# Kernel tuning notes

Measured on AMD Instinct MI355X. Metric: run time of the kernel, lower is better.

## Reference

```python
import jax, jax.numpy as jnp
import numpy as np

B, S, D = 2, 2048, 768
H = 12
HD = D // H


def setup_inputs() -> dict:
    key = jax.random.key(0)
    k1, k2, k3 = jax.random.split(key, 3)
    hidden_states = jax.random.normal(k1, (B, S, D), dtype=jnp.float32)
    Wqkv = jax.random.normal(k2, (D, 3 * D), dtype=jnp.float32) * (1.0 / np.sqrt(D))
    bqkv = jnp.zeros((3 * D,), dtype=jnp.float32)
    Wout = jax.random.normal(k3, (D, D), dtype=jnp.float32) * (1.0 / np.sqrt(D))
    bout = jnp.zeros((D,), dtype=jnp.float32)
    return {"hidden_states": hidden_states, "Wqkv": Wqkv, "bqkv": bqkv,
            "Wout": Wout, "bout": bout}


def reference(hidden_states, Wqkv, bqkv, Wout, bout):
    b, s, d = hidden_states.shape
    h, hd = H, HD
    scale = hd ** -0.5
    qkv = hidden_states @ Wqkv + bqkv                      # [b, s, 3d]
    q, k, v = jnp.split(qkv, 3, axis=-1)
    # [b, h, s, hd]
    q = q.reshape(b, s, h, hd).transpose(0, 2, 1, 3)
    k = k.reshape(b, s, h, hd).transpose(0, 2, 1, 3)
    v = v.reshape(b, s, h, hd).transpose(0, 2, 1, 3)
    scores = jnp.einsum('bhqd,bhkd->bhqk', q, k) * scale   # [b, h, s, s]
    causal = jnp.tril(jnp.ones((s, s), dtype=bool))
    scores = jnp.where(causal, scores, -jnp.inf)
    attn = jax.nn.softmax(scores, axis=-1)
    out = jnp.einsum('bhqk,bhkd->bhqd', attn, v)           # [b, h, s, hd]
    out = out.transpose(0, 2, 1, 3).reshape(b, s, d)
    return out @ Wout + bout
```

## Files before the change

kernel.cpp:

```cpp
#include <hip/hip_runtime.h>
#include <hip/hip_bf16.h>

typedef __attribute__((ext_vector_type(8))) short bf16x8;
typedef __attribute__((ext_vector_type(4))) float f32x4;
typedef __attribute__((ext_vector_type(4))) unsigned int u32x4;

#define NB 2
#define NS 2048
#define ND 768
#define NH 12
#define NHD 64
#define N3D 2304
#define NM (NB * NS)

__device__ __forceinline__ unsigned short f2bf(float x) {
    union { float f; unsigned u; } v; v.f = x;
    unsigned r = v.u + 0x7FFFu + ((v.u >> 16) & 1u);
    return (unsigned short)(r >> 16);
}

__device__ __forceinline__ unsigned cvt_pk_bf16(float lo, float hi) {
    unsigned r;
    asm volatile("v_cvt_pk_bf16_f32 %0, %1, %2" : "=v"(r) : "v"(lo), "v"(hi));
    return r;
}

__global__ __launch_bounds__(256)
void conv_bf16(const float* __restrict__ in, unsigned short* __restrict__ out) {
    const int i = (blockIdx.x * 256 + threadIdx.x) * 4;
    float4 v = *reinterpret_cast<const float4*>(in + i);
    ushort4 o;
    o.x = f2bf(v.x); o.y = f2bf(v.y); o.z = f2bf(v.z); o.w = f2bf(v.w);
    *reinterpret_cast<ushort4*>(out + i) = o;
}

__global__ __launch_bounds__(256)
void transp_conv(const float* __restrict__ in, unsigned short* __restrict__ out,
                 int K, int N) {
    __shared__ float T[32][33];
    const int n0 = blockIdx.x * 32, k0 = blockIdx.y * 32;
    const int r = threadIdx.x >> 3, c4 = (threadIdx.x & 7) * 4;
    float4 v = *reinterpret_cast<const float4*>(&in[(size_t)(k0 + r) * N + n0 + c4]);
    T[r][c4 + 0] = v.x; T[r][c4 + 1] = v.y; T[r][c4 + 2] = v.z; T[r][c4 + 3] = v.w;
    __syncthreads();
    ushort4 o;
    o.x = f2bf(T[c4 + 0][r]); o.y = f2bf(T[c4 + 1][r]);
    o.z = f2bf(T[c4 + 2][r]); o.w = f2bf(T[c4 + 3][r]);
    *reinterpret_cast<ushort4*>(&out[(size_t)(n0 + r) * K + k0 + c4]) = o;
}

template<int BM, int EPI>
__global__ __launch_bounds__(256)
void gemm_k768(const unsigned short* __restrict__ A,
               const unsigned short* __restrict__ Bt,
               const float* __restrict__ bias,
               unsigned short* __restrict__ Qo, unsigned short* __restrict__ Ko,
               unsigned short* __restrict__ Vto, float* __restrict__ Co) {
    __shared__ unsigned short As[2][BM * 64];
    __shared__ unsigned short Bs[2][128 * 64];
    const int t = threadIdx.x;
    const int wv = t >> 6, lane = t & 63;
    const int lr = lane & 15, lg = lane >> 4;
    const int wr = wv >> 1, wc = wv & 1;
    const int m0 = blockIdx.y * BM;
    const int n0 = blockIdx.x * 128;
    constexpr int FM = BM / 32;

    f32x4 acc[FM][4];
#pragma unroll
    for (int i = 0; i < FM; ++i)
#pragma unroll
        for (int j = 0; j < 4; ++j) acc[i][j] = (f32x4){0.f, 0.f, 0.f, 0.f};

    const int sr = t >> 3;
    const int sb = t & 7;

#define GSTAGE(buf, k0)                                                          \
    {                                                                            \
        _Pragma("unroll")                                                        \
        for (int jj = 0; jj < BM / 32; ++jj) {                                   \
            const int row = jj * 32 + sr;                                        \
            __builtin_amdgcn_global_load_lds(                                    \
                (const void*)(A + (size_t)(m0 + row) * ND + (k0) + ((sb ^ (row & 7)) * 8)), \
                (void*)(As[buf] + jj * 2048 + wv * 512), 16, 0, 0);              \
        }                                                                        \
        _Pragma("unroll")                                                        \
        for (int jj = 0; jj < 4; ++jj) {                                         \
            const int row = jj * 32 + sr;                                        \
            __builtin_amdgcn_global_load_lds(                                    \
                (const void*)(Bt + (size_t)(n0 + row) * ND + (k0) + ((sb ^ (row & 7)) * 8)), \
                (void*)(Bs[buf] + jj * 2048 + wv * 512), 16, 0, 0);              \
        }                                                                        \
    }

    GSTAGE(0, 0);
    for (int ki = 0; ki < ND / 64; ++ki) {
        __syncthreads();
        if (ki + 1 < ND / 64) GSTAGE((ki + 1) & 1, (ki + 1) * 64);
        const unsigned short* Ac = As[ki & 1];
        const unsigned short* Bc = Bs[ki & 1];
#pragma unroll
        for (int kc = 0; kc < 2; ++kc) {
            bf16x8 af[FM], bfr[4];
#pragma unroll
            for (int mi = 0; mi < FM; ++mi) {
                const int row = wr * (BM / 2) + mi * 16 + lr;
                af[mi] = *(const bf16x8*)&Ac[row * 64 + (((kc * 4 + lg) ^ (row & 7)) * 8)];
            }
#pragma unroll
            for (int nj = 0; nj < 4; ++nj) {
                const int row = wc * 64 + nj * 16 + lr;
                bfr[nj] = *(const bf16x8*)&Bc[row * 64 + (((kc * 4 + lg) ^ (row & 7)) * 8)];
            }
#pragma unroll
            for (int mi = 0; mi < FM; ++mi)
#pragma unroll
                for (int nj = 0; nj < 4; ++nj)
                    acc[mi][nj] = __builtin_amdgcn_mfma_f32_16x16x32_bf16(
                        af[mi], bfr[nj], acc[mi][nj], 0, 0, 0);
        }
    }
#undef GSTAGE

    if (EPI == 0) {
        const int sec = n0 / ND;
#pragma unroll
        for (int mi = 0; mi < FM; ++mi) {
#pragma unroll
            for (int nj = 0; nj < 4; ++nj) {
                const int n = n0 + wc * 64 + nj * 16 + lr;
                const int rem = n - sec * ND;
                const int hh = rem >> 6, dd = rem & 63;
                const float b = bias[n];
#pragma unroll
                for (int r = 0; r < 4; ++r) {
                    const int m = m0 + wr * (BM / 2) + mi * 16 + lg * 4 + r;
                    const int bb = m >> 11, ss = m & (NS - 1);
                    const int bhh = bb * NH + hh;
                    const float v = acc[mi][nj][r] + b;
                    if (sec == 0)
                        Qo[((size_t)bhh * NS + ss) * NHD + dd] = f2bf(v * 0.18033688011112042f);
                    else if (sec == 1)
                        Ko[((size_t)bhh * NS + ss) * NHD + dd] = f2bf(v);
                    else
                        Vto[((size_t)bhh * NHD + dd) * NS + ss] = f2bf(v);
                }
            }
        }
    } else {
#pragma unroll
        for (int mi = 0; mi < FM; ++mi)
#pragma unroll
            for (int nj = 0; nj < 4; ++nj) {
                const int n = n0 + wc * 64 + nj * 16 + lr;
                const float b = bias[n];
#pragma unroll
                for (int r = 0; r < 4; ++r) {
                    const int m = m0 + wr * (BM / 2) + mi * 16 + lg * 4 + r;
                    Co[(size_t)m * ND + n] = acc[mi][nj][r] + b;
                }
            }
    }
}

__global__ __launch_bounds__(256)
void attn_mfma(const unsigned short* __restrict__ Qg,
               const unsigned short* __restrict__ Kg,
               const unsigned short* __restrict__ Vtg,
               unsigned short* __restrict__ AO) {
    __shared__ unsigned short Ks[2][128 * 64];
    __shared__ unsigned short Vs[2][64 * 128];
    const int n = blockIdx.x;
    const int jj3 = n >> 8, cc8 = n & 255;
    const int qt = ((cc8 & 31) + jj3 * 11) & 31;
    const int bh = jj3 * 8 + (cc8 >> 5);
    const int t = threadIdx.x;
    const int w = t >> 6, lane = t & 63;
    const int lr = lane & 15, lg = lane >> 4;
    const int lgp = lg & 1;
    const int qrow = qt * 64 + w * 16 + lr;
    const size_t bhoff = (size_t)bh * (NS * NHD);

    const unsigned short* Qp = Qg + bhoff + (size_t)qrow * NHD;
    const bf16x8 qB0 = *(const bf16x8*)(Qp + lg * 8);
    const bf16x8 qB1 = *(const bf16x8*)(Qp + 32 + lg * 8);

    float m_run = -1e30f, l_part = 0.f;
    f32x4 of[4];
#pragma unroll
    for (int f = 0; f < 4; ++f) of[f] = (f32x4){0.f, 0.f, 0.f, 0.f};

    const unsigned short* Kb = Kg + bhoff;
    const unsigned short* Vb = Vtg + bhoff;
    const int ksrow = lane >> 3, ksblk = lane & 7;
    const int vsrow = lane >> 4, vsblk = lane & 15;
    const int ntiles = (qt + 2) >> 1;
    const int bswz = ((lg & 1) << 1) | (lg >> 1);

#define STAGE(buf, kv0)                                                           \
    {                                                                             \
        _Pragma("unroll")                                                         \
        for (int h = 0; h < 4; ++h) {                                             \
            const int rr = w * 32 + h * 8 + ksrow;                                \
            __builtin_amdgcn_global_load_lds(                                     \
                (const void*)(Kb + (size_t)((kv0) + rr) * NHD + ((ksblk ^ (rr & 7)) * 8)),  \
                (void*)(Ks[buf] + (w * 32 + h * 8) * 64), 16, 0, 0);              \
            const int vr = w * 16 + h * 4 + vsrow;                                \
            __builtin_amdgcn_global_load_lds(                                     \
                (const void*)(Vb + (size_t)vr * NS + (kv0) + ((vsblk ^ (vr & 7)) * 8)),     \
                (void*)(Vs[buf] + (w * 16 + h * 4) * 128), 16, 0, 0);             \
        }                                                                         \
    }

    STAGE(0, 0);
    for (int kt = 0; kt < ntiles; ++kt) {
        __syncthreads();
        if (kt + 1 < ntiles) STAGE((kt + 1) & 1, (kt + 1) * 128);
        const unsigned short* Kc = Ks[kt & 1];
        const unsigned short* Vc = Vs[kt & 1];
        const int kv0 = kt * 128;

        f32x4 sf[8];
#pragma unroll
        for (int f = 0; f < 8; ++f) sf[f] = (f32x4){0.f, 0.f, 0.f, 0.f};
        __builtin_amdgcn_s_setprio(1);
#pragma unroll
        for (int f = 0; f < 8; ++f) {
            const int krow = f * 16 + lr;
            const bf16x8 a0 = *(const bf16x8*)&Kc[krow * 64 + ((lg ^ (krow & 7)) * 8)];
            const bf16x8 a1 = *(const bf16x8*)&Kc[krow * 64 + (((4 + lg) ^ (krow & 7)) * 8)];
            sf[f] = __builtin_amdgcn_mfma_f32_16x16x32_bf16(a0, qB0, sf[f], 0, 0, 0);
            sf[f] = __builtin_amdgcn_mfma_f32_16x16x32_bf16(a1, qB1, sf[f], 0, 0, 0);
        }
        __builtin_amdgcn_s_setprio(0);

        if (kt == ntiles - 1) {
            const int thr = qrow - kv0;
#pragma unroll
            for (int f = 0; f < 8; ++f)
#pragma unroll
                for (int r = 0; r < 4; ++r)
                    if (f * 16 + lg * 4 + r > thr) sf[f][r] = -1e30f;
        }

        float tm = -1e30f;
#pragma unroll
        for (int f = 0; f < 8; ++f)
            tm = fmaxf(tm, fmaxf(fmaxf(sf[f][0], sf[f][1]), fmaxf(sf[f][2], sf[f][3])));
        tm = fmaxf(tm, __shfl_xor(tm, 16));
        tm = fmaxf(tm, __shfl_xor(tm, 32));
        if (!__all(tm <= m_run)) {
            const float nm = fmaxf(m_run, tm);
            const float corr = exp2f(m_run - nm);
            m_run = nm;
            l_part *= corr;
#pragma unroll
            for (int f = 0; f < 4; ++f)
#pragma unroll
                for (int r = 0; r < 4; ++r) of[f][r] *= corr;
        }
#pragma unroll
        for (int f = 0; f < 8; ++f)
#pragma unroll
            for (int r = 0; r < 4; ++r) {
                sf[f][r] = exp2f(sf[f][r] - m_run);
                l_part += sf[f][r];
            }

        bf16x8 pb[4];
#pragma unroll
        for (int c = 0; c < 4; ++c) {
            const unsigned A0 = cvt_pk_bf16(sf[2 * c][0], sf[2 * c][1]);
            const unsigned A1 = cvt_pk_bf16(sf[2 * c][2], sf[2 * c][3]);
            const unsigned B0 = cvt_pk_bf16(sf[2 * c + 1][0], sf[2 * c + 1][1]);
            const unsigned B1 = cvt_pk_bf16(sf[2 * c + 1][2], sf[2 * c + 1][3]);
            const unsigned s0 = lgp ? A0 : B0;
            const unsigned s1 = lgp ? A1 : B1;
            const unsigned r0 = (unsigned)__shfl_xor((int)s0, 16);
            const unsigned r1 = (unsigned)__shfl_xor((int)s1, 16);
            const unsigned o0 = lgp ? B0 : A0;
            const unsigned o1 = lgp ? B1 : A1;
            u32x4 wvv;
            wvv[0] = lgp ? r0 : o0;
            wvv[1] = lgp ? r1 : o1;
            wvv[2] = lgp ? o0 : r0;
            wvv[3] = lgp ? o1 : r1;
            pb[c] = __builtin_bit_cast(bf16x8, wvv);
        }

        __builtin_amdgcn_s_setprio(1);
#pragma unroll
        for (int fA = 0; fA < 4; ++fA) {
            const int drow = fA * 16 + lr;
#pragma unroll
            for (int c = 0; c < 4; ++c) {
                const int blk = 4 * c + bswz;
                const bf16x8 va = *(const bf16x8*)&Vc[drow * 128 + ((blk ^ (drow & 7)) * 8)];
                of[fA] = __builtin_amdgcn_mfma_f32_16x16x32_bf16(va, pb[c], of[fA], 0, 0, 0);
            }
        }
        __builtin_amdgcn_s_setprio(0);
    }
#undef STAGE

    l_part += __shfl_xor(l_part, 16);
    l_part += __shfl_xor(l_part, 32);
    const float inv = 1.f / l_part;
    const int bb = bh / NH, hh = bh - bb * NH;
    unsigned short* op = AO + ((size_t)(bb * NS + qrow)) * ND + hh * NHD;
#pragma unroll
    for (int fA = 0; fA < 4; ++fA) {
        ushort4 o4;
        o4.x = f2bf(of[fA][0] * inv);
        o4.y = f2bf(of[fA][1] * inv);
        o4.z = f2bf(of[fA][2] * inv);
        o4.w = f2bf(of[fA][3] * inv);
        *reinterpret_cast<ushort4*>(op + fA * 16 + lg * 4) = o4;
    }
}

extern "C" void kernel_launch(void* const* d_in, const int* in_sizes, int n_in,
                              void* d_out, int out_size, void* d_ws, size_t ws_size,
                              hipStream_t stream) {
    const float* hs   = (const float*)d_in[0];
    const float* Wqkv = (const float*)d_in[1];
    const float* bqkv = (const float*)d_in[2];
    const float* Wout = (const float*)d_in[3];
    const float* bout = (const float*)d_in[4];
    float* out = (float*)d_out;

    char* wp = (char*)d_ws;
    unsigned short* hsb = (unsigned short*)wp; wp += (size_t)NM * ND * 2;
    unsigned short* W1t = (unsigned short*)wp; wp += (size_t)N3D * ND * 2;
    unsigned short* W2t = (unsigned short*)wp; wp += (size_t)ND * ND * 2;
    const size_t per = (size_t)NB * NH * NS * NHD;
    unsigned short* Qb  = (unsigned short*)wp; wp += per * 2;
    unsigned short* Kb  = (unsigned short*)wp; wp += per * 2;
    unsigned short* Vtb = (unsigned short*)wp; wp += per * 2;
    unsigned short* AOb = (unsigned short*)wp; wp += per * 2;

    conv_bf16<<<(NM * ND) / 1024, 256, 0, stream>>>(hs, hsb);
    transp_conv<<<dim3(N3D / 32, ND / 32), 256, 0, stream>>>(Wqkv, W1t, ND, N3D);
    transp_conv<<<dim3(ND / 32, ND / 32), 256, 0, stream>>>(Wout, W2t, ND, ND);

    gemm_k768<128, 0><<<dim3(N3D / 128, NM / 128), 256, 0, stream>>>(
        hsb, W1t, bqkv, Qb, Kb, Vtb, nullptr);

    attn_mfma<<<dim3(NS / 64 * NB * NH), 256, 0, stream>>>(Qb, Kb, Vtb, AOb);

    gemm_k768<64, 1><<<dim3(ND / 128, NM / 64), 256, 0, stream>>>(
        AOb, W2t, bout, nullptr, nullptr, nullptr, out);
}
```

Measured before the change: 191.3 us.

## Write V row-major then transpose separately; retile out-proj GEMM; reorder attention blocks

The QKV GEMM epilogue now writes V in the same row-major [bh,s,d] layout as Q and K, reusing the AO buffer as scratch. A new vtransp kernel then transposes it through LDS into the Vt layout with vectorized stores, replacing the strided scattered 2-byte stores. The output projection GEMM moves from 64x128 to 64x64 tiles, doubling its block count. The attention block-to-(head, q-tile) mapping is also changed so adjacent blocks take different heads and heavy causal tiles are scheduled first, at the cost of an extra kernel launch and a round trip of V through memory.

```diff
diff --git a/kernel.cpp b/kernel.cpp
--- a/kernel.cpp
+++ b/kernel.cpp
@@ -49,28 +49,52 @@
     *reinterpret_cast<ushort4*>(&out[(size_t)(n0 + r) * K + k0 + c4]) = o;
 }
 
-template<int BM, int EPI>
+__global__ __launch_bounds__(256)
+void vtransp(const unsigned short* __restrict__ V, unsigned short* __restrict__ Vt) {
+    __shared__ __align__(16) unsigned short T[64][72];
+    const int bh = blockIdx.y;
+    const int s0 = blockIdx.x * 64;
+    const int t = threadIdx.x;
+    const unsigned short* src = V + ((size_t)bh * NS + s0) * NHD;
+    const int r = t >> 2, cc = (t & 3) * 16;
+    *(bf16x8*)&T[r][cc]     = *(const bf16x8*)&src[r * NHD + cc];
+    *(bf16x8*)&T[r][cc + 8] = *(const bf16x8*)&src[r * NHD + cc + 8];
+    __syncthreads();
+    unsigned short* dst = Vt + ((size_t)bh * NHD) * NS + s0;
+    const int chunk = t & 7;
+#pragma unroll
+    for (int h = 0; h < 2; ++h) {
+        const int d = (t >> 3) + h * 32;
+        bf16x8 v;
+#pragma unroll
+        for (int e = 0; e < 8; ++e) v[e] = (short)T[chunk * 8 + e][d];
+        *(bf16x8*)&dst[(size_t)d * NS + chunk * 8] = v;
+    }
+}
+
+template<int BM, int BN, int EPI>
 __global__ __launch_bounds__(256)
 void gemm_k768(const unsigned short* __restrict__ A,
                const unsigned short* __restrict__ Bt,
                const float* __restrict__ bias,
                unsigned short* __restrict__ Qo, unsigned short* __restrict__ Ko,
-               unsigned short* __restrict__ Vto, float* __restrict__ Co) {
+               unsigned short* __restrict__ Vo, float* __restrict__ Co) {
     __shared__ unsigned short As[2][BM * 64];
-    __shared__ unsigned short Bs[2][128 * 64];
+    __shared__ unsigned short Bs[2][BN * 64];
     const int t = threadIdx.x;
     const int wv = t >> 6, lane = t & 63;
     const int lr = lane & 15, lg = lane >> 4;
     const int wr = wv >> 1, wc = wv & 1;
     const int m0 = blockIdx.y * BM;
-    const int n0 = blockIdx.x * 128;
+    const int n0 = blockIdx.x * BN;
     constexpr int FM = BM / 32;
-
-    f32x4 acc[FM][4];
+    constexpr int FN = BN / 32;
+
+    f32x4 acc[FM][FN];
 #pragma unroll
     for (int i = 0; i < FM; ++i)
 #pragma unroll
-        for (int j = 0; j < 4; ++j) acc[i][j] = (f32x4){0.f, 0.f, 0.f, 0.f};
+        for (int j = 0; j < FN; ++j) acc[i][j] = (f32x4){0.f, 0.f, 0.f, 0.f};
 
     const int sr = t >> 3;
     const int sb = t & 7;
@@ -85,7 +109,7 @@
                 (void*)(As[buf] + jj * 2048 + wv * 512), 16, 0, 0);              \
         }                                                                        \
         _Pragma("unroll")                                                        \
-        for (int jj = 0; jj < 4; ++jj) {                                         \
+        for (int jj = 0; jj < BN / 32; ++jj) {                                   \
             const int row = jj * 32 + sr;                                        \
             __builtin_amdgcn_global_load_lds(                                    \
                 (const void*)(Bt + (size_t)(n0 + row) * ND + (k0) + ((sb ^ (row & 7)) * 8)), \
@@ -101,21 +125,21 @@
         const unsigned short* Bc = Bs[ki & 1];
 #pragma unroll
         for (int kc = 0; kc < 2; ++kc) {
-            bf16x8 af[FM], bfr[4];
+            bf16x8 af[FM], bfr[FN];
 #pragma unroll
             for (int mi = 0; mi < FM; ++mi) {
                 const int row = wr * (BM / 2) + mi * 16 + lr;
                 af[mi] = *(const bf16x8*)&Ac[row * 64 + (((kc * 4 + lg) ^ (row & 7)) * 8)];
             }
 #pragma unroll
-            for (int nj = 0; nj < 4; ++nj) {
-                const int row = wc * 64 + nj * 16 + lr;
+            for (int nj = 0; nj < FN; ++nj) {
+                const int row = wc * (BN / 2) + nj * 16 + lr;
                 bfr[nj] = *(const bf16x8*)&Bc[row * 64 + (((kc * 4 + lg) ^ (row & 7)) * 8)];
             }
 #pragma unroll
             for (int mi = 0; mi < FM; ++mi)
 #pragma unroll
-                for (int nj = 0; nj < 4; ++nj)
+                for (int nj = 0; nj < FN; ++nj)
                     acc[mi][nj] = __builtin_amdgcn_mfma_f32_16x16x32_bf16(
                         af[mi], bfr[nj], acc[mi][nj], 0, 0, 0);
         }
@@ -127,8 +151,8 @@
 #pragma unroll
         for (int mi = 0; mi < FM; ++mi) {
 #pragma unroll
-            for (int nj = 0; nj < 4; ++nj) {
-                const int n = n0 + wc * 64 + nj * 16 + lr;
+            for (int nj = 0; nj < FN; ++nj) {
+                const int n = n0 + wc * (BN / 2) + nj * 16 + lr;
                 const int rem = n - sec * ND;
                 const int hh = rem >> 6, dd = rem & 63;
                 const float b = bias[n];
@@ -143,7 +167,7 @@
                     else if (sec == 1)
                         Ko[((size_t)bhh * NS + ss) * NHD + dd] = f2bf(v);
                     else
-                        Vto[((size_t)bhh * NHD + dd) * NS + ss] = f2bf(v);
+                        Vo[((size_t)bhh * NS + ss) * NHD + dd] = f2bf(v);
                 }
             }
         }
@@ -151,8 +175,8 @@
 #pragma unroll
         for (int mi = 0; mi < FM; ++mi)
 #pragma unroll
-            for (int nj = 0; nj < 4; ++nj) {
-                const int n = n0 + wc * 64 + nj * 16 + lr;
+            for (int nj = 0; nj < FN; ++nj) {
+                const int n = n0 + wc * (BN / 2) + nj * 16 + lr;
                 const float b = bias[n];
 #pragma unroll
                 for (int r = 0; r < 4; ++r) {
@@ -171,9 +195,9 @@
     __shared__ unsigned short Ks[2][128 * 64];
     __shared__ unsigned short Vs[2][64 * 128];
     const int n = blockIdx.x;
-    const int jj3 = n >> 8, cc8 = n & 255;
-    const int qt = ((cc8 & 31) + jj3 * 11) & 31;
-    const int bh = jj3 * 8 + (cc8 >> 5);
+    const int x = n & 7, ii = n >> 3;
+    const int bh = ((ii >> 5) << 3) + x;
+    const int qt = (31 - (ii & 31) + 11 * (ii >> 5)) & 31;
     const int t = threadIdx.x;
     const int w = t >> 6, lane = t & 63;
     const int lr = lane & 15, lg = lane >> 4;
@@ -343,11 +367,13 @@
     transp_conv<<<dim3(N3D / 32, ND / 32), 256, 0, stream>>>(Wqkv, W1t, ND, N3D);
     transp_conv<<<dim3(ND / 32, ND / 32), 256, 0, stream>>>(Wout, W2t, ND, ND);
 
-    gemm_k768<128, 0><<<dim3(N3D / 128, NM / 128), 256, 0, stream>>>(
-        hsb, W1t, bqkv, Qb, Kb, Vtb, nullptr);
+    gemm_k768<128, 128, 0><<<dim3(N3D / 128, NM / 128), 256, 0, stream>>>(
+        hsb, W1t, bqkv, Qb, Kb, AOb, nullptr);
+
+    vtransp<<<dim3(NS / 64, NB * NH), 256, 0, stream>>>(AOb, Vtb);
 
     attn_mfma<<<dim3(NS / 64 * NB * NH), 256, 0, stream>>>(Qb, Kb, Vtb, AOb);
 
-    gemm_k768<64, 1><<<dim3(ND / 128, NM / 64), 256, 0, stream>>>(
+    gemm_k768<64, 64, 1><<<dim3(ND / 64, NM / 64), 256, 0, stream>>>(
         AOb, W2t, bout, nullptr, nullptr, nullptr, out);
 }
```

After: 192.6 us. About the same (+0.7%).
